# Performance work log

Measured on AMD Instinct MI355X. Metric: run time of the kernel, lower is better.

Reference implementation:

```python
import jax, jax.numpy as jnp
import numpy as np

EPS = 1e-12  # F.normalize default eps

def l2norm(x, axis=1):
    n = jnp.sqrt(jnp.sum(x * x, axis=axis, keepdims=True))
    return x / jnp.maximum(n, EPS)

def setup_inputs() -> dict:
    key = jax.random.key(0)
    ks = jax.random.split(key, 8)
    N, C, H, W = 32, 1024, 28, 28
    D, K, OUT = 128, 64, 1024
    return {
        "x": jax.random.normal(ks[0], (N, C, H, W), dtype=jnp.float32),
        "Wpool": jax.random.normal(ks[1], (D, C), dtype=jnp.float32) * 0.02,
        "bpool": jax.random.normal(ks[2], (D,), dtype=jnp.float32) * 0.02,
        "Wconv": jax.random.normal(ks[3], (K, D), dtype=jnp.float32) * 0.1,
        "bconv": jax.random.normal(ks[4], (K,), dtype=jnp.float32) * 0.02,
        "centroids": jax.random.uniform(ks[5], (K, D), dtype=jnp.float32),
        "Wproj": jax.random.normal(ks[6], (OUT, K * D), dtype=jnp.float32) * 0.02,
        "bproj": jax.random.normal(ks[7], (OUT,), dtype=jnp.float32) * 0.02,
    }

def reference(x, Wpool, bpool, Wconv, bconv, centroids, Wproj, bproj):
    N, C, H, W = x.shape
    K, D = centroids.shape
    S = H * W
    # 1x1 conv channel pool: (N,C,H,W) -> (N,D,H,W)
    x = jnp.einsum('nchw,dc->ndhw', x, Wpool) + bpool[None, :, None, None]
    # descriptor-wise L2 norm over channel dim
    x = l2norm(x, axis=1)
    xf = x.reshape(N, D, S)                      # (N,D,S)
    # 1x1 conv -> soft assignment logits, softmax over clusters
    sa = jnp.einsum('nds,kd->nks', xf, Wconv) + bconv[None, :, None]
    sa = jax.nn.softmax(sa, axis=1)              # (N,K,S)
    # vlad[n,k,d] = sum_s sa[n,k,s]*(xf[n,d,s] - centroids[k,d])
    #            = (sa @ xf^T) - centroids * sum_s sa   (GEMM rewrite, same math)
    vlad = jnp.einsum('nks,nds->nkd', sa, xf) - centroids[None] * jnp.sum(sa, axis=-1)[:, :, None]
    vlad = l2norm(vlad, axis=1)                  # L2Norm over dim=1 (clusters)
    vlad = vlad.reshape(N, K * D)
    vlad = vlad @ Wproj.T + bproj
    return l2norm(vlad, axis=1)
```

## Files before the change

kernel.cpp:

```cpp
#include <hip/hip_runtime.h>
#include <math.h>

#define NB 32
#define CC 1024
#define SS 784
#define SP 832
#define DD 128
#define KK 64
#define OUTD 1024
#define KD 8192
#define NSPLIT 13
#define PSPLIT 32

#define OFF_XN    0
#define OFF_SA    (OFF_XN + NB*DD*SP*2)
#define OFF_WPK   (OFF_SA + NB*KK*SP*2)
#define OFF_WCK   (OFF_WPK + 32*8*64*8*2)
#define OFF_VLADP (OFF_WCK + 16*64*8*2)
#define OFF_SASUM (OFF_VLADP + NB*NSPLIT*KD*4)
#define OFF_VLADN (OFF_SASUM + NB*NSPLIT*KK*4)
#define OFF_OUTP  (OFF_VLADN + NB*KD*4)

typedef __attribute__((ext_vector_type(8))) short bf16x8;
typedef __attribute__((ext_vector_type(4))) float f32x4;

__device__ __forceinline__ unsigned int pk_bf16(float a, float b) {
    unsigned int ua = __builtin_bit_cast(unsigned int, a);
    unsigned int ub = __builtin_bit_cast(unsigned int, b);
    ua += 0x7FFFu + ((ua >> 16) & 1u);
    ub += 0x7FFFu + ((ub >> 16) & 1u);
    return (ua >> 16) | (ub & 0xFFFF0000u);
}
__device__ __forceinline__ unsigned short f2bf(float a) {
    unsigned int ua = __builtin_bit_cast(unsigned int, a);
    ua += 0x7FFFu + ((ua >> 16) & 1u);
    return (unsigned short)(ua >> 16);
}
__device__ __forceinline__ float bf2f(unsigned short u) {
    unsigned int v = ((unsigned int)u) << 16;
    return __builtin_bit_cast(float, v);
}

__global__ __launch_bounds__(256)
void pack_weights(const float* __restrict__ Wpool, const float* __restrict__ Wconv,
                  unsigned short* __restrict__ Wpk, unsigned short* __restrict__ Wck)
{
    const int b = blockIdx.x;
    const int t = threadIdx.x;
    if (b < 8) {
#pragma unroll
        for (int i = 0; i < 8; i++) {
            const int id = t + 256 * i;
            const int ktl = id >> 9;
            const int mt  = (id >> 6) & 7;
            const int l   = id & 63;
            const int lm = l & 15, quad = l >> 4;
            const int kt = b * 4 + ktl;
            const int d = mt * 16 + lm;
            const int c = kt * 32 + quad * 8;
            const float4 v0 = *(const float4*)&Wpool[(size_t)d * CC + c];
            const float4 v1 = *(const float4*)&Wpool[(size_t)d * CC + c + 4];
            unsigned int* dst = (unsigned int*)&Wpk[(size_t)((kt * 8 + mt) * 64 + l) * 8];
            dst[0] = pk_bf16(v0.x, v0.y); dst[1] = pk_bf16(v0.z, v0.w);
            dst[2] = pk_bf16(v1.x, v1.y); dst[3] = pk_bf16(v1.z, v1.w);
        }
    } else {
#pragma unroll
        for (int i = 0; i < 4; i++) {
            const int id = t + 256 * i;
            const int tile = id >> 6;
            const int l = id & 63;
            const int lm = l & 15, quad = l >> 4;
            const int k = (tile >> 2) * 16 + lm;
            const int d = (tile & 3) * 32 + quad * 8;
            const float4 v0 = *(const float4*)&Wconv[(size_t)k * DD + d];
            const float4 v1 = *(const float4*)&Wconv[(size_t)k * DD + d + 4];
            unsigned int* dst = (unsigned int*)&Wck[(size_t)(tile * 64 + l) * 8];
            dst[0] = pk_bf16(v0.x, v0.y); dst[1] = pk_bf16(v0.z, v0.w);
            dst[2] = pk_bf16(v1.x, v1.y); dst[3] = pk_bf16(v1.z, v1.w);
        }
    }
}

__global__ __launch_bounds__(256)
void pool_norm_assign(const float* __restrict__ x, const unsigned short* __restrict__ Wpk,
                      const float* __restrict__ bpool, const unsigned short* __restrict__ Wck,
                      const float* __restrict__ bconv,
                      unsigned short* __restrict__ xn, unsigned short* __restrict__ sa)
{
    const int n  = blockIdx.y;
    const int s0 = blockIdx.x * 16;
    const int t  = threadIdx.x;
    const int l  = t & 63;
    const int w  = t >> 6;
    const int lm = l & 15;
    const int quad = l >> 4;

    __shared__ alignas(16) unsigned short Bst[128 * 16 * 8];
    __shared__ alignas(16) unsigned short xnT[16 * 16 * 8];
    __shared__ float red[4][16];
    __shared__ float sums[4][16];

    {
        const int s_l = t & 15;
        const int cb0 = t >> 4;
        const int sg  = s0 + s_l;
        const int s_c = (sg < SS) ? sg : (SS - 1);
        const float* xb = x + (size_t)n * CC * SS + s_c;
#pragma unroll
        for (int it = 0; it < 8; it++) {
            const int cblk = cb0 + 16 * it;
            const float* xp = xb + (size_t)(cblk * 8) * SS;
            float v[8];
#pragma unroll
            for (int j = 0; j < 8; j++) v[j] = xp[(size_t)j * SS];
            unsigned int* dst = (unsigned int*)&Bst[(size_t)(cblk * 16 + s_l) * 8];
            dst[0] = pk_bf16(v[0], v[1]); dst[1] = pk_bf16(v[2], v[3]);
            dst[2] = pk_bf16(v[4], v[5]); dst[3] = pk_bf16(v[6], v[7]);
        }
    }
    __syncthreads();

    f32x4 acc[2];
    acc[0] = (f32x4){0.f, 0.f, 0.f, 0.f};
    acc[1] = (f32x4){0.f, 0.f, 0.f, 0.f};

    bf16x8 a_nxt[2];
#pragma unroll
    for (int i = 0; i < 2; i++)
        a_nxt[i] = *(const bf16x8*)&Wpk[(size_t)((0 * 8 + w * 2 + i) * 64 + l) * 8];

    for (int kt = 0; kt < 32; kt++) {
        const bf16x8 a0 = a_nxt[0], a1 = a_nxt[1];
        if (kt < 31) {
#pragma unroll
            for (int i = 0; i < 2; i++)
                a_nxt[i] = *(const bf16x8*)&Wpk[(size_t)(((kt + 1) * 8 + w * 2 + i) * 64 + l) * 8];
        }
        const bf16x8 bfrag = *(const bf16x8*)&Bst[(size_t)((kt * 4 + quad) * 16 + lm) * 8];
        acc[0] = __builtin_amdgcn_mfma_f32_16x16x32_bf16(a0, bfrag, acc[0], 0, 0, 0);
        acc[1] = __builtin_amdgcn_mfma_f32_16x16x32_bf16(a1, bfrag, acc[1], 0, 0, 0);
    }

    float vals[2][4];
    float ssq = 0.f;
#pragma unroll
    for (int i = 0; i < 2; i++)
#pragma unroll
        for (int r = 0; r < 4; r++) {
            const int d = (w * 2 + i) * 16 + quad * 4 + r;
            const float v = acc[i][r] + bpool[d];
            vals[i][r] = v; ssq += v * v;
        }
    ssq += __shfl_xor(ssq, 16, 64);
    ssq += __shfl_xor(ssq, 32, 64);
    if (quad == 0) red[w][lm] = ssq;
    __syncthreads();
    const float scale = 1.f / fmaxf(sqrtf(red[0][lm] + red[1][lm] + red[2][lm] + red[3][lm]), 1e-12f);
    const int sg = s0 + lm;
    unsigned short* xnp = xn + (size_t)n * DD * SP;
#pragma unroll
    for (int i = 0; i < 2; i++)
#pragma unroll
        for (int r = 0; r < 4; r++) {
            const int d = (w * 2 + i) * 16 + quad * 4 + r;
            const float v = vals[i][r] * scale;
            xnp[(size_t)d * SP + sg] = f2bf(v);
            xnT[(size_t)(((d >> 3) * 16) + lm) * 8 + (d & 7)] = f2bf(v);
        }
    __syncthreads();

    f32x4 acc2 = (f32x4){0.f, 0.f, 0.f, 0.f};
#pragma unroll
    for (int dsv = 0; dsv < 4; dsv++) {
        const bf16x8 bfrag = *(const bf16x8*)&xnT[(size_t)((dsv * 4 + quad) * 16 + lm) * 8];
        const bf16x8 afrag = *(const bf16x8*)&Wck[(size_t)((w * 4 + dsv) * 64 + l) * 8];
        acc2 = __builtin_amdgcn_mfma_f32_16x16x32_bf16(afrag, bfrag, acc2, 0, 0, 0);
    }
    float e[4]; float ps = 0.f;
#pragma unroll
    for (int r = 0; r < 4; r++) {
        const int k = w * 16 + quad * 4 + r;
        e[r] = expf(acc2[r] + bconv[k]);
        ps += e[r];
    }
    ps += __shfl_xor(ps, 16, 64);
    ps += __shfl_xor(ps, 32, 64);
    if (quad == 0) sums[w][lm] = ps;
    __syncthreads();
    const float inv = 1.f / (sums[0][lm] + sums[1][lm] + sums[2][lm] + sums[3][lm]);
    const bool val2 = sg < SS;
    unsigned short* sap = sa + (size_t)n * KK * SP;
#pragma unroll
    for (int r = 0; r < 4; r++) {
        const int k = w * 16 + quad * 4 + r;
        sap[(size_t)k * SP + sg] = val2 ? f2bf(e[r] * inv) : (unsigned short)0;
    }
}

__global__ __launch_bounds__(256)
void vlad_mfma(const unsigned short* __restrict__ xn, const unsigned short* __restrict__ sa,
               float* __restrict__ vladp, float* __restrict__ sasump)
{
    const int p = blockIdx.x;
    const int n = blockIdx.y;
    const int t = threadIdx.x;
    const int l = t & 63;
    const int w = t >> 6;
    const int kth = w & 1, nh = w >> 1;
    const int lm = l & 15, quad = l >> 4;

    const unsigned short* sap = sa + (size_t)n * KK * SP;
    const unsigned short* xnp = xn + (size_t)n * DD * SP;

    f32x4 acc[2][4];
#pragma unroll
    for (int j = 0; j < 2; j++)
#pragma unroll
        for (int i = 0; i < 4; i++) acc[j][i] = (f32x4){0.f, 0.f, 0.f, 0.f};

#pragma unroll
    for (int st = 0; st < 2; st++) {
        const int sb = p * 64 + st * 32 + quad * 8;
        bf16x8 af[2], bfv[4];
#pragma unroll
        for (int j = 0; j < 2; j++)
            af[j] = *(const bf16x8*)&sap[(size_t)((kth * 2 + j) * 16 + lm) * SP + sb];
#pragma unroll
        for (int i = 0; i < 4; i++)
            bfv[i] = *(const bf16x8*)&xnp[(size_t)((nh * 4 + i) * 16 + lm) * SP + sb];
#pragma unroll
        for (int j = 0; j < 2; j++)
#pragma unroll
            for (int i = 0; i < 4; i++)
                acc[j][i] = __builtin_amdgcn_mfma_f32_16x16x32_bf16(af[j], bfv[i], acc[j][i], 0, 0, 0);
    }

    float* vp = vladp + ((size_t)n * NSPLIT + p) * KD;
#pragma unroll
    for (int j = 0; j < 2; j++)
#pragma unroll
        for (int i = 0; i < 4; i++) {
            const int kq = (kth * 2 + j) * 4 + quad;
            const int d  = (nh * 4 + i) * 16 + lm;
            *(f32x4*)&vp[(size_t)(kq * DD + d) * 4] = acc[j][i];
        }

    if (t < KK) {
        float sm = 0.f;
        const unsigned short* rp = &sap[(size_t)t * SP + p * 64];
#pragma unroll
        for (int c = 0; c < 64; c++) sm += bf2f(rp[c]);
        sasump[((size_t)n * NSPLIT + p) * KK + t] = sm;
    }
}

__global__ __launch_bounds__(256)
void vlad_finish(const float* __restrict__ vladp, const float* __restrict__ sasump,
                 const float* __restrict__ centroids, float* __restrict__ vladn)
{
    const int dg = blockIdx.x;
    const int n  = blockIdx.y;
    const int t  = threadIdx.x;
    const int kq = t & 15;
    const int d  = dg * 16 + (t >> 4);

    __shared__ float sas[KK];
    if (t < KK) {
        float sm = 0.f;
#pragma unroll
        for (int p = 0; p < NSPLIT; p++) sm += sasump[((size_t)n * NSPLIT + p) * KK + t];
        sas[t] = sm;
    }
    __syncthreads();

    f32x4 v = (f32x4){0.f, 0.f, 0.f, 0.f};
#pragma unroll
    for (int p = 0; p < NSPLIT; p++) {
        const f32x4 pr = *(const f32x4*)&vladp[((size_t)n * NSPLIT + p) * KD + (size_t)(kq * DD + d) * 4];
        v += pr;
    }
#pragma unroll
    for (int r = 0; r < 4; r++)
        v[r] -= centroids[(size_t)(kq * 4 + r) * DD + d] * sas[kq * 4 + r];

    float ssq = v[0] * v[0] + v[1] * v[1] + v[2] * v[2] + v[3] * v[3];
    ssq += __shfl_xor(ssq, 1, 64);
    ssq += __shfl_xor(ssq, 2, 64);
    ssq += __shfl_xor(ssq, 4, 64);
    ssq += __shfl_xor(ssq, 8, 64);
    const float scale = 1.f / fmaxf(sqrtf(ssq), 1e-12f);

    float* vo = vladn + (size_t)n * KD;
#pragma unroll
    for (int r = 0; r < 4; r++)
        vo[(size_t)(kq * 4 + r) * DD + d] = v[r] * scale;
}

__global__ __launch_bounds__(256)
void proj_mfma(const float* __restrict__ vladn, const float* __restrict__ Wproj,
               float* __restrict__ outp)
{
    const int o0 = blockIdx.x * 64;
    const int c0 = blockIdx.y * (KD / PSPLIT);
    const int t  = threadIdx.x;
    const int l  = t & 63;
    const int w  = t >> 6;
    const int lm = l & 15, quad = l >> 4;
    const int o  = o0 + w * 16 + lm;

    f32x4 acc[2];
    acc[0] = (f32x4){0.f, 0.f, 0.f, 0.f};
    acc[1] = (f32x4){0.f, 0.f, 0.f, 0.f};

#pragma unroll 2
    for (int kt = 0; kt < 8; kt++) {
        const int c = c0 + kt * 32 + quad * 8;
        const float4 b0 = *(const float4*)&Wproj[(size_t)o * KD + c];
        const float4 b1 = *(const float4*)&Wproj[(size_t)o * KD + c + 4];
        float4 a00 = *(const float4*)&vladn[(size_t)(0 * 16 + lm) * KD + c];
        float4 a01 = *(const float4*)&vladn[(size_t)(0 * 16 + lm) * KD + c + 4];
        float4 a10 = *(const float4*)&vladn[(size_t)(16 + lm) * KD + c];
        float4 a11 = *(const float4*)&vladn[(size_t)(16 + lm) * KD + c + 4];
        union { unsigned int u[4]; bf16x8 v; } ub, ua0, ua1;
        ub.u[0] = pk_bf16(b0.x, b0.y); ub.u[1] = pk_bf16(b0.z, b0.w);
        ub.u[2] = pk_bf16(b1.x, b1.y); ub.u[3] = pk_bf16(b1.z, b1.w);
        ua0.u[0] = pk_bf16(a00.x, a00.y); ua0.u[1] = pk_bf16(a00.z, a00.w);
        ua0.u[2] = pk_bf16(a01.x, a01.y); ua0.u[3] = pk_bf16(a01.z, a01.w);
        ua1.u[0] = pk_bf16(a10.x, a10.y); ua1.u[1] = pk_bf16(a10.z, a10.w);
        ua1.u[2] = pk_bf16(a11.x, a11.y); ua1.u[3] = pk_bf16(a11.z, a11.w);
        acc[0] = __builtin_amdgcn_mfma_f32_16x16x32_bf16(ua0.v, ub.v, acc[0], 0, 0, 0);
        acc[1] = __builtin_amdgcn_mfma_f32_16x16x32_bf16(ua1.v, ub.v, acc[1], 0, 0, 0);
    }

#pragma unroll
    for (int a = 0; a < 2; a++)
#pragma unroll
        for (int r = 0; r < 4; r++) {
            const int nn = a * 16 + quad * 4 + r;
            outp[((size_t)blockIdx.y * NB + nn) * OUTD + o] = acc[a][r];
        }
}

__global__ __launch_bounds__(256)
void final_norm_kernel(const float* __restrict__ outp, const float* __restrict__ bproj,
                       float* __restrict__ out)
{
    const int n = blockIdx.x;
    const int t = threadIdx.x;
    const int o4 = t * 4;

    float4 a = *(const float4*)&bproj[o4];
#pragma unroll
    for (int p = 0; p < PSPLIT; p++) {
        const float4 pr = *(const float4*)&outp[((size_t)p * NB + n) * OUTD + o4];
        a.x += pr.x; a.y += pr.y; a.z += pr.z; a.w += pr.w;
    }
    float ssp = a.x * a.x + a.y * a.y + a.z * a.z + a.w * a.w;
#pragma unroll
    for (int off = 32; off > 0; off >>= 1) ssp += __shfl_down(ssp, off, 64);
    __shared__ float rs[4];
    if ((t & 63) == 0) rs[t >> 6] = ssp;
    __syncthreads();
    const float total = rs[0] + rs[1] + rs[2] + rs[3];
    const float scale = 1.f / fmaxf(sqrtf(total), 1e-12f);
    float4 o;
    o.x = a.x * scale; o.y = a.y * scale; o.z = a.z * scale; o.w = a.w * scale;
    *(float4*)&out[(size_t)n * OUTD + o4] = o;
}

extern "C" void kernel_launch(void* const* d_in, const int* in_sizes, int n_in,
                              void* d_out, int out_size, void* d_ws, size_t ws_size,
                              hipStream_t stream)
{
    const float* x         = (const float*)d_in[0];
    const float* Wpool     = (const float*)d_in[1];
    const float* bpool     = (const float*)d_in[2];
    const float* Wconv     = (const float*)d_in[3];
    const float* bconv     = (const float*)d_in[4];
    const float* centroids = (const float*)d_in[5];
    const float* Wproj     = (const float*)d_in[6];
    const float* bproj     = (const float*)d_in[7];
    float* out = (float*)d_out;
    char*  wsb = (char*)d_ws;

    unsigned short* xn     = (unsigned short*)(wsb + OFF_XN);
    unsigned short* sa     = (unsigned short*)(wsb + OFF_SA);
    unsigned short* Wpk    = (unsigned short*)(wsb + OFF_WPK);
    unsigned short* Wck    = (unsigned short*)(wsb + OFF_WCK);
    float*          vladp  = (float*)(wsb + OFF_VLADP);
    float*          sasump = (float*)(wsb + OFF_SASUM);
    float*          vladn  = (float*)(wsb + OFF_VLADN);
    float*          outp   = (float*)(wsb + OFF_OUTP);

    pack_weights<<<dim3(9), 256, 0, stream>>>(Wpool, Wconv, Wpk, Wck);
    pool_norm_assign<<<dim3(SP / 16, NB), 256, 0, stream>>>(x, Wpk, bpool, Wck, bconv, xn, sa);
    vlad_mfma<<<dim3(NSPLIT, NB), 256, 0, stream>>>(xn, sa, vladp, sasump);
    vlad_finish<<<dim3(DD / 16, NB), 256, 0, stream>>>(vladp, sasump, centroids, vladn);
    proj_mfma<<<dim3(OUTD / 64, PSPLIT), 256, 0, stream>>>(vladn, Wproj, outp);
    final_norm_kernel<<<dim3(NB), 256, 0, stream>>>(outp, bproj, out);
}
```

Measured before the change: 233.0 us.

## Vectorize x loads, halve LDS staging with two-phase pipelined loads, swizzle

In the pool kernel, each thread now loads four consecutive spatial positions of x as float4 instead of scalar strided loads. The channel dimension is staged through LDS in two halves, and the second half's global loads are issued before the first half's MFMA loop so they overlap with compute. The halved LDS buffer uses an XOR swizzle to reduce bank conflicts, and launch bounds request higher occupancy. Padded tiles beyond the spatial extent now just write zeros and exit, and the sa-sum loop uses 16-byte vector loads. The extra register buffer for the second half may raise register pressure against the occupancy hint.

```diff
diff --git a/kernel.cpp b/kernel.cpp
--- a/kernel.cpp
+++ b/kernel.cpp
@@ -23,6 +23,7 @@
 
 typedef __attribute__((ext_vector_type(8))) short bf16x8;
 typedef __attribute__((ext_vector_type(4))) float f32x4;
+typedef __attribute__((ext_vector_type(4))) unsigned int u32x4;
 
 __device__ __forceinline__ unsigned int pk_bf16(float a, float b) {
     unsigned int ua = __builtin_bit_cast(unsigned int, a);
@@ -82,7 +83,7 @@
     }
 }
 
-__global__ __launch_bounds__(256)
+__global__ __launch_bounds__(256, 6)
 void pool_norm_assign(const float* __restrict__ x, const unsigned short* __restrict__ Wpk,
                       const float* __restrict__ bpool, const unsigned short* __restrict__ Wck,
                       const float* __restrict__ bconv,
@@ -96,30 +97,50 @@
     const int lm = l & 15;
     const int quad = l >> 4;
 
-    __shared__ alignas(16) unsigned short Bst[128 * 16 * 8];
+    __shared__ alignas(16) unsigned short Bst[64 * 16 * 8];
     __shared__ alignas(16) unsigned short xnT[16 * 16 * 8];
     __shared__ float red[4][16];
     __shared__ float sums[4][16];
 
+    unsigned short* xnp = xn + (size_t)n * DD * SP;
+    unsigned short* sap = sa + (size_t)n * KK * SP;
+
+    if (s0 >= SS) {
+        const u32x4 z = (u32x4){0u, 0u, 0u, 0u};
+        const int d  = t >> 1;
+        const int hh = t & 1;
+        *(u32x4*)&xnp[(size_t)d * SP + s0 + hh * 8] = z;
+        if (t < 128) {
+            const int k = t >> 1;
+            *(u32x4*)&sap[(size_t)k * SP + s0 + hh * 8] = z;
+        }
+        return;
+    }
+
+    const int oct   = t >> 2;
+    const int squad = t & 3;
+    const int s_l4  = squad * 4;
+    const float* xbase = x + (size_t)n * CC * SS + s0 + s_l4;
+
     {
-        const int s_l = t & 15;
-        const int cb0 = t >> 4;
-        const int sg  = s0 + s_l;
-        const int s_c = (sg < SS) ? sg : (SS - 1);
-        const float* xb = x + (size_t)n * CC * SS + s_c;
-#pragma unroll
-        for (int it = 0; it < 8; it++) {
-            const int cblk = cb0 + 16 * it;
-            const float* xp = xb + (size_t)(cblk * 8) * SS;
-            float v[8];
-#pragma unroll
-            for (int j = 0; j < 8; j++) v[j] = xp[(size_t)j * SS];
-            unsigned int* dst = (unsigned int*)&Bst[(size_t)(cblk * 16 + s_l) * 8];
-            dst[0] = pk_bf16(v[0], v[1]); dst[1] = pk_bf16(v[2], v[3]);
-            dst[2] = pk_bf16(v[4], v[5]); dst[3] = pk_bf16(v[6], v[7]);
-        }
-    }
-    __syncthreads();
+        f32x4 f[8];
+#pragma unroll
+        for (int j = 0; j < 8; j++)
+            f[j] = *(const f32x4*)&xbase[(size_t)(oct * 8 + j) * SS];
+#pragma unroll
+        for (int ss = 0; ss < 4; ss++) {
+            const int s = s_l4 + ss;
+            unsigned int* dst = (unsigned int*)&Bst[(size_t)(oct * 16 + (s ^ (oct & 7))) * 8];
+            dst[0] = pk_bf16(f[0][ss], f[1][ss]); dst[1] = pk_bf16(f[2][ss], f[3][ss]);
+            dst[2] = pk_bf16(f[4][ss], f[5][ss]); dst[3] = pk_bf16(f[6][ss], f[7][ss]);
+        }
+    }
+    __syncthreads();
+
+    f32x4 g[8];
+#pragma unroll
+    for (int j = 0; j < 8; j++)
+        g[j] = *(const f32x4*)&xbase[(size_t)(512 + oct * 8 + j) * SS];
 
     f32x4 acc[2];
     acc[0] = (f32x4){0.f, 0.f, 0.f, 0.f};
@@ -130,14 +151,36 @@
     for (int i = 0; i < 2; i++)
         a_nxt[i] = *(const bf16x8*)&Wpk[(size_t)((0 * 8 + w * 2 + i) * 64 + l) * 8];
 
-    for (int kt = 0; kt < 32; kt++) {
+    for (int kt = 0; kt < 16; kt++) {
+        const bf16x8 a0 = a_nxt[0], a1 = a_nxt[1];
+#pragma unroll
+        for (int i = 0; i < 2; i++)
+            a_nxt[i] = *(const bf16x8*)&Wpk[(size_t)(((kt + 1) * 8 + w * 2 + i) * 64 + l) * 8];
+        const int cb = kt * 4 + quad;
+        const bf16x8 bfrag = *(const bf16x8*)&Bst[(size_t)(cb * 16 + (lm ^ (cb & 7))) * 8];
+        acc[0] = __builtin_amdgcn_mfma_f32_16x16x32_bf16(a0, bfrag, acc[0], 0, 0, 0);
+        acc[1] = __builtin_amdgcn_mfma_f32_16x16x32_bf16(a1, bfrag, acc[1], 0, 0, 0);
+    }
+    __syncthreads();
+
+#pragma unroll
+    for (int ss = 0; ss < 4; ss++) {
+        const int s = s_l4 + ss;
+        unsigned int* dst = (unsigned int*)&Bst[(size_t)(oct * 16 + (s ^ (oct & 7))) * 8];
+        dst[0] = pk_bf16(g[0][ss], g[1][ss]); dst[1] = pk_bf16(g[2][ss], g[3][ss]);
+        dst[2] = pk_bf16(g[4][ss], g[5][ss]); dst[3] = pk_bf16(g[6][ss], g[7][ss]);
+    }
+    __syncthreads();
+
+    for (int kt = 16; kt < 32; kt++) {
         const bf16x8 a0 = a_nxt[0], a1 = a_nxt[1];
         if (kt < 31) {
 #pragma unroll
             for (int i = 0; i < 2; i++)
                 a_nxt[i] = *(const bf16x8*)&Wpk[(size_t)(((kt + 1) * 8 + w * 2 + i) * 64 + l) * 8];
         }
-        const bf16x8 bfrag = *(const bf16x8*)&Bst[(size_t)((kt * 4 + quad) * 16 + lm) * 8];
+        const int cb = (kt & 15) * 4 + quad;
+        const bf16x8 bfrag = *(const bf16x8*)&Bst[(size_t)(cb * 16 + (lm ^ (cb & 7))) * 8];
         acc[0] = __builtin_amdgcn_mfma_f32_16x16x32_bf16(a0, bfrag, acc[0], 0, 0, 0);
         acc[1] = __builtin_amdgcn_mfma_f32_16x16x32_bf16(a1, bfrag, acc[1], 0, 0, 0);
     }
@@ -158,7 +201,6 @@
     __syncthreads();
     const float scale = 1.f / fmaxf(sqrtf(red[0][lm] + red[1][lm] + red[2][lm] + red[3][lm]), 1e-12f);
     const int sg = s0 + lm;
-    unsigned short* xnp = xn + (size_t)n * DD * SP;
 #pragma unroll
     for (int i = 0; i < 2; i++)
 #pragma unroll
@@ -189,12 +231,10 @@
     if (quad == 0) sums[w][lm] = ps;
     __syncthreads();
     const float inv = 1.f / (sums[0][lm] + sums[1][lm] + sums[2][lm] + sums[3][lm]);
-    const bool val2 = sg < SS;
-    unsigned short* sap = sa + (size_t)n * KK * SP;
 #pragma unroll
     for (int r = 0; r < 4; r++) {
         const int k = w * 16 + quad * 4 + r;
-        sap[(size_t)k * SP + sg] = val2 ? f2bf(e[r] * inv) : (unsigned short)0;
+        sap[(size_t)k * SP + sg] = f2bf(e[r] * inv);
     }
 }
 
@@ -250,7 +290,11 @@
         float sm = 0.f;
         const unsigned short* rp = &sap[(size_t)t * SP + p * 64];
 #pragma unroll
-        for (int c = 0; c < 64; c++) sm += bf2f(rp[c]);
+        for (int c8 = 0; c8 < 8; c8++) {
+            const bf16x8 v = *(const bf16x8*)&rp[c8 * 8];
+#pragma unroll
+            for (int j = 0; j < 8; j++) sm += bf2f((unsigned short)v[j]);
+        }
         sasump[((size_t)n * NSPLIT + p) * KK + t] = sm;
     }
 }
```

Result: no change. 232.1 us (-0.4%).
